# Kernel tuning notes

Hardware: AMD Instinct MI355X
Metric: run time of the kernel (lower is better)

## Reference

```python
import jax, jax.numpy as jnp
import numpy as np

UNITS = 2048
BATCH = 4096
INPUT_DIM = 2048

def hard_sigmoid(x):
    # Keras hard_sigmoid: clip(0.2*x + 0.5, 0, 1)
    return jnp.clip(0.2 * x + 0.5, 0.0, 1.0)

def setup_inputs() -> dict:
    key = jax.random.key(0)
    ks = jax.random.split(key, 8)
    inputs = jax.random.normal(ks[0], (BATCH, INPUT_DIM), dtype=jnp.float32)
    h_tm1 = jax.random.normal(ks[1], (BATCH, UNITS), dtype=jnp.float32)
    c_tm1 = jax.random.normal(ks[2], (BATCH, UNITS), dtype=jnp.float32)
    z_tm1 = jax.random.normal(ks[3], (BATCH, UNITS), dtype=jnp.float32)
    scale = 1.0 / np.sqrt(INPUT_DIM)
    kernel = jax.random.normal(ks[4], (INPUT_DIM, 4 * UNITS), dtype=jnp.float32) * scale
    recurrent_kernel = jax.random.normal(ks[5], (UNITS, 4 * UNITS), dtype=jnp.float32) * scale
    recurrent_latent = jax.random.normal(ks[6], (UNITS, 4 * UNITS), dtype=jnp.float32) * scale
    # unit_forget_bias: bias = [zeros(units), ones(units), zeros(2*units)]
    bias = jnp.concatenate([
        jnp.zeros((UNITS,), jnp.float32),
        jnp.ones((UNITS,), jnp.float32),
        jnp.zeros((2 * UNITS,), jnp.float32),
    ])
    return {"inputs": inputs, "h_tm1": h_tm1, "c_tm1": c_tm1, "z_tm1": z_tm1,
            "kernel": kernel, "recurrent_kernel": recurrent_kernel,
            "recurrent_latent": recurrent_latent, "bias": bias}

def reference(inputs, h_tm1, c_tm1, z_tm1, kernel, recurrent_kernel, recurrent_latent, bias):
    # Fused path (implementation=2, no dropout): three matmuls + bias,
    # split into 4 gates, then gated state update.
    x = inputs @ kernel + h_tm1 @ recurrent_kernel + z_tm1 @ recurrent_latent + bias
    x_i, x_f, x_c, x_o = jnp.split(x, 4, axis=1)
    i = hard_sigmoid(x_i)
    f = hard_sigmoid(x_f)
    c = f * c_tm1 + i * jnp.tanh(x_c)
    o = hard_sigmoid(x_o)
    h = o * jnp.tanh(c)
    return h
```

## Files before the change

kernel.cpp:

```cpp
#include <hip/hip_runtime.h>
#include <hip/hip_bf16.h>

typedef float f32x4 __attribute__((ext_vector_type(4)));
typedef short short8 __attribute__((ext_vector_type(8)));
typedef short short4v __attribute__((ext_vector_type(4)));

__device__ __forceinline__ short f2b(float x) {
    union { __hip_bfloat16 b; short s; } u;
    u.b = __float2bfloat16(x);
    return u.s;
}

__device__ __forceinline__ void gload16(const void* g, void* l) {
    __builtin_amdgcn_global_load_lds(
        (const __attribute__((address_space(1))) unsigned int*)g,
        (__attribute__((address_space(3))) unsigned int*)l, 16, 0, 0);
}

__global__ __launch_bounds__(256)
void conv_a(const float* __restrict__ x0, const float* __restrict__ x1,
            const float* __restrict__ x2, unsigned short* __restrict__ Aws)
{
    const long i = (long)blockIdx.x * 256 + threadIdx.x;
    const long per_src = (long)4096 * 2048 / 8;
    const int  s = (int)(i / per_src);
    const long e0 = (i % per_src) * 8;
    const int  row = (int)(e0 >> 11), kl = (int)(e0 & 2047);
    const float* src = (s == 0) ? x0 : (s == 1) ? x1 : x2;
    const f32x4 v0 = *(const f32x4*)(src + e0);
    const f32x4 v1 = *(const f32x4*)(src + e0 + 4);
    short8 p;
    #pragma unroll
    for (int j = 0; j < 4; ++j) { p[j] = f2b(v0[j]); p[4 + j] = f2b(v1[j]); }
    *(short8*)&Aws[(long)row * 6144 + s * 2048 + kl] = p;
}

__global__ __launch_bounds__(256)
void conv_b(const float* __restrict__ Wk, const float* __restrict__ Wr,
            const float* __restrict__ Wl, unsigned short* __restrict__ Bws)
{
    __shared__ float lt[64][65];
    const int bid = (int)blockIdx.x;
    const int s   = bid >> 12;
    const int r   = bid & 4095;
    const int kbase = (r >> 7) * 64;
    const int ebase = (r & 127) * 64;
    const float* W = (s == 0) ? Wk : (s == 1) ? Wr : Wl;
    const int tr = threadIdx.x >> 4, tc = threadIdx.x & 15;

    #pragma unroll
    for (int p = 0; p < 4; ++p) {
        const int kr = p * 16 + tr;
        const f32x4 v = *(const f32x4*)&W[(long)(kbase + kr) * 8192 + ebase + tc * 4];
        #pragma unroll
        for (int j = 0; j < 4; ++j) lt[kr][tc * 4 + j] = v[j];
    }
    __syncthreads();
    #pragma unroll
    for (int p = 0; p < 4; ++p) {
        const int er = p * 16 + tr;
        const int k4 = tc * 4;
        short4v qv;
        #pragma unroll
        for (int j = 0; j < 4; ++j) qv[j] = f2b(lt[k4 + j][er]);
        *(short4v*)&Bws[(long)(ebase + er) * 6144 + (long)s * 2048 + kbase + k4] = qv;
    }
}

__global__ __launch_bounds__(256, 2)
void vlstm_gemm8(const unsigned short* __restrict__ Aws,
                 const unsigned short* __restrict__ Bws,
                 const float* __restrict__ c_tm1,
                 const float* __restrict__ bias,
                 float* __restrict__ out)
{
    __shared__ __align__(16) unsigned short lds[2][2][128][64];

    const int tid  = threadIdx.x;
    const int w    = tid >> 6, lane = tid & 63;
    const int wm   = w >> 1,  wn   = w & 1;
    const int l15  = lane & 15, q = lane >> 4;
    const int lrow = lane >> 3;
    const int lsw  = (lane & 7) ^ lrow;
    const int oq   = q ^ (l15 & 7);

    const int bid = (int)blockIdx.x;
    const int swz = (bid & 7) * 256 + (bid >> 3);
    const int bm  = swz >> 6, bn = swz & 63;
    const int row0 = bm * 128, c0 = bn * 32;

    const long a_src0 = (long)(row0 + w * 32 + lrow) * 6144 + lsw * 8;
    const long b_src0 = (long)(c0 + w * 8 + lrow) * 6144 + lsw * 8;

    f32x4 acc[4][4];
    #pragma unroll
    for (int mi = 0; mi < 4; ++mi)
        #pragma unroll
        for (int g = 0; g < 4; ++g)
            acc[mi][g] = (f32x4){0.f, 0.f, 0.f, 0.f};

    short8 afr[4][2];
    short8 bfr[4][2];

#define STAGE_A(buf_, t_) do { _Pragma("unroll")                                 \
    for (int j_ = 0; j_ < 4; ++j_)                                               \
        gload16(Aws + a_src0 + (long)j_ * (8 * 6144) + (t_) * 64,                \
                &lds[buf_][0][w * 32 + j_ * 8][0]); } while (0)

#define STAGE_B(buf_, t_) do { _Pragma("unroll")                                 \
    for (int j_ = 0; j_ < 4; ++j_)    \
        gload16(Bws + b_src0 + (long)j_ * (2048 * 6144) + (t_) * 64,             \
                &lds[buf_][1][j_ * 32 + w * 8][0]); } while (0)

#define LOAD_AFR(cur_) do { _Pragma("unroll")                                    \
    for (int mi_ = 0; mi_ < 4; ++mi_) { _Pragma("unroll")                        \
        for (int h_ = 0; h_ < 2; ++h_)                                           \
            afr[mi_][h_] = *(const short8*)                                      \
                &lds[cur_][0][wm * 64 + mi_ * 16 + l15][(oq ^ (h_ << 2)) * 8];   \
    } } while (0)

#define LOAD_BFR(cur_, glo_) do { _Pragma("unroll")                              \
    for (int g_ = 0; g_ < 2; ++g_) { _Pragma("unroll")                           \
        for (int h_ = 0; h_ < 2; ++h_)                                           \
            bfr[(glo_) + g_][h_] = *(const short8*)                              \
                &lds[cur_][1][((glo_) + g_) * 32 + wn * 16 + l15]                \
                             [(oq ^ (h_ << 2)) * 8];                             \
    } } while (0)

#define MFMA_Q(glo_) do {                                                        \
    __builtin_amdgcn_s_setprio(1);                                               \
    _Pragma("unroll")                                                            \
    for (int h_ = 0; h_ < 2; ++h_) { _Pragma("unroll")                           \
        for (int mi_ = 0; mi_ < 4; ++mi_) { _Pragma("unroll")                    \
            for (int g_ = 0; g_ < 2; ++g_)                                       \
                acc[mi_][(glo_) + g_] = __builtin_amdgcn_mfma_f32_16x16x32_bf16( \
                    afr[mi_][h_], bfr[(glo_) + g_][h_], acc[mi_][(glo_) + g_],   \
                    0, 0, 0); } }                                                \
    __builtin_amdgcn_s_setprio(0); } while (0)

    STAGE_A(0, 0);
    STAGE_B(0, 0);
    asm volatile("s_waitcnt vmcnt(0)" ::: "memory");
    __builtin_amdgcn_s_barrier();
    __builtin_amdgcn_sched_barrier(0);

    for (int t = 0; t < 95; ++t) {
        const int cur = t & 1;
        STAGE_A(cur ^ 1, t + 1);
        LOAD_AFR(cur);
        LOAD_BFR(cur, 0);
        MFMA_Q(0);
        asm volatile("s_waitcnt vmcnt(4)" ::: "memory");
        __builtin_amdgcn_s_barrier();
        __builtin_amdgcn_sched_barrier(0);
        STAGE_B(cur ^ 1, t + 1);
        LOAD_BFR(cur, 2);
        MFMA_Q(2);
        asm volatile("s_waitcnt vmcnt(2)" ::: "memory");
        __builtin_amdgcn_s_barrier();
        __builtin_amdgcn_sched_barrier(0);
    }
    {
        const int cur = 95 & 1;
        LOAD_AFR(cur);
        LOAD_BFR(cur, 0);
        MFMA_Q(0);
        asm volatile("s_waitcnt vmcnt(0)" ::: "memory");
        __builtin_amdgcn_s_barrier();
        __builtin_amdgcn_sched_barrier(0);
        LOAD_BFR(cur, 2);
        MFMA_Q(2);
    }

#undef STAGE_A
#undef STAGE_B
#undef LOAD_AFR
#undef LOAD_BFR
#undef MFMA_Q

    {
        const int col = c0 + wn * 16 + l15;
        const float bi  = bias[col];
        const float bf_ = bias[2048 + col];
        const float bc  = bias[4096 + col];
        const float bo  = bias[6144 + col];
        #pragma unroll
        for (int mi = 0; mi < 4; ++mi) {
            const int rbase = row0 + wm * 64 + mi * 16 + q * 4;
            #pragma unroll
            for (int rr = 0; rr < 4; ++rr) {
                const int row = rbase + rr;
                const float xi = acc[mi][0][rr] + bi;
                const float xf = acc[mi][1][rr] + bf_;
                const float xc = acc[mi][2][rr] + bc;
                const float xo = acc[mi][3][rr] + bo;
                const float ig = __builtin_amdgcn_fmed3f(0.2f * xi + 0.5f, 0.f, 1.f);
                const float fg = __builtin_amdgcn_fmed3f(0.2f * xf + 0.5f, 0.f, 1.f);
                const float og = __builtin_amdgcn_fmed3f(0.2f * xo + 0.5f, 0.f, 1.f);
                const float cp = c_tm1[(long)row * 2048 + col];
                const float cc = fg * cp + ig * tanhf(xc);
                out[(long)row * 2048 + col] = og * tanhf(cc);
            }
        }
    }
}

__global__ __launch_bounds__(256, 2)
void vlstm_fused_legacy(const float* __restrict__ xin, const float* __restrict__ h_tm1,
                        const float* __restrict__ c_tm1, const float* __restrict__ z_tm1,
                        const float* __restrict__ Wk, const float* __restrict__ Wr,
                        const float* __restrict__ Wl, const float* __restrict__ bias,
                        float* __restrict__ out)
{
    __shared__ __align__(16) unsigned short Alds[2][128][40];
    __shared__ __align__(16) unsigned short Blds[2][256][40];

    const int tid  = threadIdx.x;
    const int wave = tid >> 6, lane = tid & 63;
    const int wr = wave >> 1, wc = wave & 1;
    const int l15 = lane & 15, q = lane >> 4;

    const int bid = (int)blockIdx.x;
    const int swz = (bid & 7) * 128 + (bid >> 3);
    const int bm = swz >> 5, bn = swz & 31;
    const int row0 = bm * 128, col0 = bn * 64;

    const int arow = tid >> 1, kh = tid & 1;
    const long bg_off = (long)(tid >> 6) * 2048 + col0 + (tid & 63);

    f32x4 acc[4][4][2];
    #pragma unroll
    for (int g = 0; g < 4; ++g)
        #pragma unroll
        for (int mi = 0; mi < 4; ++mi)
            #pragma unroll
            for (int ni = 0; ni < 2; ++ni)
                acc[g][mi][ni] = (f32x4){0.f, 0.f, 0.f, 0.f};

    f32x4 sa[4];
    float sb[32];

#define DO_LOADS_L(kn_) do {                                                    \
    const int s_  = (kn_) >> 6;                                                 \
    const int kl_ = ((kn_) & 63) << 5;                                          \
    const float* Ap_ = (s_ == 0) ? xin : (s_ == 1) ? h_tm1 : z_tm1;             \
    const float* Bp_ = (s_ == 0) ? Wk  : (s_ == 1) ? Wr    : Wl;                \
    const float* ap_ = Ap_ + (long)(row0 + arow) * 2048 + kl_ + kh * 16;        \
    _Pragma("unroll")                                                           \
    for (int i_ = 0; i_ < 4; ++i_) sa[i_] = ((const f32x4*)ap_)[i_];            \
    const float* bp_ = Bp_ + (long)kl_ * 8192 + bg_off;                         \
    _Pragma("unroll")                                                           \
    for (int kk_ = 0; kk_ < 32; ++kk_) sb[kk_] = bp_[(long)kk_ * 8192];         \
} while (0)

#define DO_STORE_L(buf_) do {                                                   \
    short8 p0_, p1_;                                                            \
    _Pragma("unroll")                                                           \
    for (int j_ = 0; j_ < 4; ++j_) {                                            \
        p0_[j_] = f2b(sa[0][j_]); p0_[4 + j_] = f2b(sa[1][j_]);                 \
        p1_[j_] = f2b(sa[2][j_]); p1_[4 + j_] = f2b(sa[3][j_]);                 \
    }                                                                           \
    *(short8*)&Alds[buf_][arow][kh * 16]     = p0_;                             \
    *(short8*)&Alds[buf_][arow][kh * 16 + 8] = p1_;                             \
    _Pragma("unroll")                                                           \
    for (int ks_ = 0; ks_ < 4; ++ks_) {                                         \
        short8 pb_;                                                             \
        _Pragma("unroll")                                                       \
        for (int j_ = 0; j_ < 8; ++j_) pb_[j_] = f2b(sb[ks_ * 8 + j_]);         \
        *(short8*)&Blds[buf_][tid][ks_ * 8] = pb_;                              \
    }                                                                           \
} while (0)

    DO_LOADS_L(0);
    DO_STORE_L(0);
    __syncthreads();

    for (int kt = 0; kt < 192; ++kt) {
        const int cur = kt & 1;
        if (kt + 1 < 192) DO_LOADS_L(kt + 1);

        short8 afr[4];
        #pragma unroll
        for (int mi = 0; mi < 4; ++mi)
            afr[mi] = *(const short8*)&Alds[cur][wr * 64 + mi * 16 + l15][q * 8];

        short8 bfr[4][2];
        #pragma unroll
        for (int g = 0; g < 4; ++g)
            #pragma unroll
            for (int ni = 0; ni < 2; ++ni)
                bfr[g][ni] = *(const short8*)
                    &Blds[cur][g * 64 + wc * 32 + ni * 16 + l15][q * 8];

        #pragma unroll
        for (int g = 0; g < 4; ++g)
            #pragma unroll
            for (int ni = 0; ni < 2; ++ni)
                #pragma unroll
                for (int mi = 0; mi < 4; ++mi)
                    acc[g][mi][ni] = __builtin_amdgcn_mfma_f32_16x16x32_bf16(
                        afr[mi], bfr[g][ni], acc[g][mi][ni], 0, 0, 0);

        if (kt + 1 < 192) DO_STORE_L(cur ^ 1);
        __syncthreads();
    }

#undef DO_LOADS_L
#undef DO_STORE_L

    #pragma unroll
    for (int ni = 0; ni < 2; ++ni) {
        const int col = col0 + wc * 32 + ni * 16 + l15;
        const float bi  = bias[col];
        const float bf_ = bias[2048 + col];
        const float bc  = bias[4096 + col];
        const float bo  = bias[6144 + col];
        #pragma unroll
        for (int mi = 0; mi < 4; ++mi) {
            const int rbase = row0 + wr * 64 + mi * 16 + q * 4;
            #pragma unroll
            for (int rr = 0; rr < 4; ++rr) {
                const int row = rbase + rr;
                const float xi = acc[0][mi][ni][rr] + bi;
                const float xf = acc[1][mi][ni][rr] + bf_;
                const float xc = acc[2][mi][ni][rr] + bc;
                const float xo = acc[3][mi][ni][rr] + bo;
                const float ig = __builtin_amdgcn_fmed3f(0.2f * xi + 0.5f, 0.f, 1.f);
                const float fg = __builtin_amdgcn_fmed3f(0.2f * xf + 0.5f, 0.f, 1.f);
                const float og = __builtin_amdgcn_fmed3f(0.2f * xo + 0.5f, 0.f, 1.f);
                const float cp = c_tm1[(long)row * 2048 + col];
                const float cc = fg * cp + ig * tanhf(xc);
                out[(long)row * 2048 + col] = og * tanhf(cc);
            }
        }
    }
}

extern "C" void kernel_launch(void* const* d_in, const int* in_sizes, int n_in,
                              void* d_out, int out_size, void* d_ws, size_t ws_size,
                              hipStream_t stream) {
    const float* xin  = (const float*)d_in[0];
    const float* h1   = (const float*)d_in[1];
    const float* c1   = (const float*)d_in[2];
    const float* z1   = (const float*)d_in[3];
    const float* Wk   = (const float*)d_in[4];
    const float* Wr   = (const float*)d_in[5];
    const float* Wl   = (const float*)d_in[6];
    const float* bias = (const float*)d_in[7];
    float* out = (float*)d_out;
    (void)in_sizes; (void)n_in; (void)out_size;

    const size_t a_elems = (size_t)4096 * 6144;
    const size_t b_elems = (size_t)8192 * 6144;
    const size_t need = (a_elems + b_elems) * 2;

    if (ws_size >= need) {
        unsigned short* Aws = (unsigned short*)d_ws;
        unsigned short* Bws = Aws + a_elems;
        conv_a<<<dim3(12288), dim3(256), 0, stream>>>(xin, h1, z1, Aws);
        conv_b<<<dim3(12288), dim3(256), 0, stream>>>(Wk, Wr, Wl, Bws);
        vlstm_gemm8<<<dim3(2048), dim3(256), 0, stream>>>(Aws, Bws, c1, bias, out);
    } else {
        vlstm_fused_legacy<<<dim3(1024), dim3(256), 0, stream>>>(
            xin, h1, c1, z1, Wk, Wr, Wl, bias, out);
    }
}
```

Baseline: 552.0 us.

## Enlarge GEMM tile to 256x256 with 8 waves and phased LDS pipeline

Replaces the 128-row by 32-unit (128 gate columns) block tile with a 256-row by 64-unit (256 gate columns) tile, run by 512 threads in 8 waves, each wave owning a 128x64 sub-tile. Staging of A and B into LDS is split across four barrier-delimited phases, and B is prefetched two iterations ahead. The aim is to raise arithmetic intensity and cut global/L2 traffic per MFMA. In exchange it uses more registers (acc[8][4]), LDS and barriers, and the launch drops to 512 blocks, which may hurt occupancy and load balance.

```diff
diff --git a/kernel.cpp b/kernel.cpp
--- a/kernel.cpp
+++ b/kernel.cpp
@@ -67,34 +67,34 @@
     }
 }
 
-__global__ __launch_bounds__(256, 2)
-void vlstm_gemm8(const unsigned short* __restrict__ Aws,
-                 const unsigned short* __restrict__ Bws,
-                 const float* __restrict__ c_tm1,
-                 const float* __restrict__ bias,
-                 float* __restrict__ out)
+__global__ __launch_bounds__(512, 2)
+void vlstm_gemm256(const unsigned short* __restrict__ Aws,
+                   const unsigned short* __restrict__ Bws,
+                   const float* __restrict__ c_tm1,
+                   const float* __restrict__ bias,
+                   float* __restrict__ out)
 {
-    __shared__ __align__(16) unsigned short lds[2][2][128][64];
+    __shared__ __align__(16) unsigned short As[2][256][64];
+    __shared__ __align__(16) unsigned short Bs[2][256][64];
 
     const int tid  = threadIdx.x;
     const int w    = tid >> 6, lane = tid & 63;
-    const int wm   = w >> 1,  wn   = w & 1;
+    const int wm   = w >> 2,  wn   = w & 3;
     const int l15  = lane & 15, q = lane >> 4;
     const int lrow = lane >> 3;
     const int lsw  = (lane & 7) ^ lrow;
     const int oq   = q ^ (l15 & 7);
 
     const int bid = (int)blockIdx.x;
-    const int swz = (bid & 7) * 256 + (bid >> 3);
-    const int bm  = swz >> 6, bn = swz & 63;
-    const int row0 = bm * 128, c0 = bn * 32;
-
-    const long a_src0 = (long)(row0 + w * 32 + lrow) * 6144 + lsw * 8;
-    const long b_src0 = (long)(c0 + w * 8 + lrow) * 6144 + lsw * 8;
-
-    f32x4 acc[4][4];
-    #pragma unroll
-    for (int mi = 0; mi < 4; ++mi)
+    const int swz = (bid & 7) * 64 + (bid >> 3);
+    const int bm  = swz >> 5, bn = swz & 31;
+    const int row0 = bm * 256, c0 = bn * 64;
+
+    const long a_base = (long)(row0 + w * 16 + lrow) * 6144 + lsw * 8;
+
+    f32x4 acc[8][4];
+    #pragma unroll
+    for (int mi = 0; mi < 8; ++mi)
         #pragma unroll
         for (int g = 0; g < 4; ++g)
             acc[mi][g] = (f32x4){0.f, 0.f, 0.f, 0.f};
@@ -102,74 +102,84 @@
     short8 afr[4][2];
     short8 bfr[4][2];
 
-#define STAGE_A(buf_, t_) do { _Pragma("unroll")                                 \
-    for (int j_ = 0; j_ < 4; ++j_)                                               \
-        gload16(Aws + a_src0 + (long)j_ * (8 * 6144) + (t_) * 64,                \
-                &lds[buf_][0][w * 32 + j_ * 8][0]); } while (0)
-
-#define STAGE_B(buf_, t_) do { _Pragma("unroll")                                 \
-    for (int j_ = 0; j_ < 4; ++j_)    \
-        gload16(Bws + b_src0 + (long)j_ * (2048 * 6144) + (t_) * 64,             \
-                &lds[buf_][1][j_ * 32 + w * 8][0]); } while (0)
-
-#define LOAD_AFR(cur_) do { _Pragma("unroll")                                    \
+#define STAGE_A(buf_, t_, h_) do { _Pragma("unroll")                             \
+    for (int j_ = 0; j_ < 2; ++j_)                                               \
+        gload16(Aws + a_base + (long)((h_) * 128 + j_ * 8) * 6144                \
+                    + (long)(t_) * 64,                                           \
+                &As[buf_][(h_) * 128 + w * 16 + j_ * 8][0]); } while (0)
+
+#define STAGE_B(buf_, t_, h_) do { _Pragma("unroll")                             \
+    for (int j_ = 0; j_ < 2; ++j_) {                                             \
+        const int e0_ = (h_) * 128 + w * 16 + j_ * 8;                            \
+        const int grow_ = ((e0_ >> 4) & 3) * 2048 + c0 + (e0_ >> 6) * 16         \
+                          + (e0_ & 8) + lrow;                                    \
+        gload16(Bws + (long)grow_ * 6144 + lsw * 8 + (long)(t_) * 64,            \
+                &Bs[buf_][e0_][0]); } } while (0)
+
+#define LOAD_AFR(cur_, mh_) do { _Pragma("unroll")                               \
     for (int mi_ = 0; mi_ < 4; ++mi_) { _Pragma("unroll")                        \
-        for (int h_ = 0; h_ < 2; ++h_)                                           \
-            afr[mi_][h_] = *(const short8*)                                      \
-                &lds[cur_][0][wm * 64 + mi_ * 16 + l15][(oq ^ (h_ << 2)) * 8];   \
-    } } while (0)
-
-#define LOAD_BFR(cur_, glo_) do { _Pragma("unroll")                              \
+        for (int kh_ = 0; kh_ < 2; ++kh_)                                        \
+            afr[mi_][kh_] = *(const short8*)                                     \
+                &As[cur_][wm * 128 + (mh_) * 64 + mi_ * 16 + l15]                \
+                         [(oq ^ (kh_ << 2)) * 8]; } } while (0)
+
+#define LOAD_BFR(cur_, nlo_) do { _Pragma("unroll")                              \
     for (int g_ = 0; g_ < 2; ++g_) { _Pragma("unroll")                           \
-        for (int h_ = 0; h_ < 2; ++h_)                                           \
-            bfr[(glo_) + g_][h_] = *(const short8*)                              \
-                &lds[cur_][1][((glo_) + g_) * 32 + wn * 16 + l15]                \
-                             [(oq ^ (h_ << 2)) * 8];                             \
-    } } while (0)
-
-#define MFMA_Q(glo_) do {                                                        \
+        for (int kh_ = 0; kh_ < 2; ++kh_)                                        \
+            bfr[(nlo_) + g_][kh_] = *(const short8*)                             \
+                &Bs[cur_][wn * 64 + ((nlo_) + g_) * 16 + l15]                    \
+                         [(oq ^ (kh_ << 2)) * 8]; } } while (0)
+
+#define MFMA_Q(mh_, nlo_) do {                                                   \
     __builtin_amdgcn_s_setprio(1);                                               \
     _Pragma("unroll")                                                            \
-    for (int h_ = 0; h_ < 2; ++h_) { _Pragma("unroll")                           \
+    for (int kh_ = 0; kh_ < 2; ++kh_) { _Pragma("unroll")                        \
         for (int mi_ = 0; mi_ < 4; ++mi_) { _Pragma("unroll")                    \
             for (int g_ = 0; g_ < 2; ++g_)                                       \
-                acc[mi_][(glo_) + g_] = __builtin_amdgcn_mfma_f32_16x16x32_bf16( \
-                    afr[mi_][h_], bfr[(glo_) + g_][h_], acc[mi_][(glo_) + g_],   \
-                    0, 0, 0); } }                                                \
+                acc[(mh_) * 4 + mi_][(nlo_) + g_] =                              \
+                    __builtin_amdgcn_mfma_f32_16x16x32_bf16(                     \
+                        afr[mi_][kh_], bfr[(nlo_) + g_][kh_],                    \
+                        acc[(mh_) * 4 + mi_][(nlo_) + g_], 0, 0, 0); } }         \
     __builtin_amdgcn_s_setprio(0); } while (0)
 
-    STAGE_A(0, 0);
-    STAGE_B(0, 0);
-    asm volatile("s_waitcnt vmcnt(0)" ::: "memory");
+#define PH_OPEN() do { __builtin_amdgcn_s_barrier();                             \
+    asm volatile("s_waitcnt lgkmcnt(0)" ::: "memory");                           \
+    __builtin_amdgcn_sched_barrier(0); } while (0)
+
+#define PH_CLOSE() do { __builtin_amdgcn_s_barrier();                            \
+    __builtin_amdgcn_sched_barrier(0); } while (0)
+
+    STAGE_A(0, 0, 0); STAGE_A(0, 0, 1);
+    STAGE_B(0, 0, 0); STAGE_B(0, 0, 1);
+    STAGE_B(1, 1, 0); STAGE_B(1, 1, 1);
+    asm volatile("s_waitcnt vmcnt(4)" ::: "memory");
     __builtin_amdgcn_s_barrier();
     __builtin_amdgcn_sched_barrier(0);
 
-    for (int t = 0; t < 95; ++t) {
-        const int cur = t & 1;
-        STAGE_A(cur ^ 1, t + 1);
-        LOAD_AFR(cur);
+    for (int t = 0; t < 96; ++t) {
+        const int cur = t & 1, nxt = cur ^ 1;
+        LOAD_AFR(cur, 0);
         LOAD_BFR(cur, 0);
-        MFMA_Q(0);
-        asm volatile("s_waitcnt vmcnt(4)" ::: "memory");
-        __builtin_amdgcn_s_barrier();
-        __builtin_amdgcn_sched_barrier(0);
-        STAGE_B(cur ^ 1, t + 1);
+        if (t + 1 < 96) STAGE_A(nxt, t + 1, 0);
+        PH_OPEN();
+        MFMA_Q(0, 0);
+        PH_CLOSE();
         LOAD_BFR(cur, 2);
-        MFMA_Q(2);
-        asm volatile("s_waitcnt vmcnt(2)" ::: "memory");
-        __builtin_amdgcn_s_barrier();
-        __builtin_amdgcn_sched_barrier(0);
-    }
-    {
-        const int cur = 95 & 1;
-        LOAD_AFR(cur);
-        LOAD_BFR(cur, 0);
-        MFMA_Q(0);
-        asm volatile("s_waitcnt vmcnt(0)" ::: "memory");
-        __builtin_amdgcn_s_barrier();
-        __builtin_amdgcn_sched_barrier(0);
-        LOAD_BFR(cur, 2);
-        MFMA_Q(2);
+        if (t + 1 < 96) STAGE_A(nxt, t + 1, 1);
+        PH_OPEN();
+        MFMA_Q(0, 2);
+        PH_CLOSE();
+        LOAD_AFR(cur, 1);
+        if (t + 2 < 96) STAGE_B(cur, t + 2, 0);
+        PH_OPEN();
+        MFMA_Q(1, 0);
+        PH_CLOSE();
+        if (t + 2 < 96) STAGE_B(cur, t + 2, 1);
+        PH_OPEN();
+        MFMA_Q(1, 2);
+        if (t < 94) asm volatile("s_waitcnt vmcnt(4)" ::: "memory");
+        else        asm volatile("s_waitcnt vmcnt(0)" ::: "memory");
+        PH_CLOSE();
     }
 
 #undef STAGE_A
@@ -177,6 +187,8 @@
 #undef LOAD_AFR
 #undef LOAD_BFR
 #undef MFMA_Q
+#undef PH_OPEN
+#undef PH_CLOSE
 
     {
         const int col = c0 + wn * 16 + l15;
@@ -185,8 +197,8 @@
         const float bc  = bias[4096 + col];
         const float bo  = bias[6144 + col];
         #pragma unroll
-        for (int mi = 0; mi < 4; ++mi) {
-            const int rbase = row0 + wm * 64 + mi * 16 + q * 4;
+        for (int mi = 0; mi < 8; ++mi) {
+            const int rbase = row0 + wm * 128 + mi * 16 + q * 4;
             #pragma unroll
             for (int rr = 0; rr < 4; ++rr) {
                 const int row = rbase + rr;
@@ -359,7 +371,7 @@
         unsigned short* Bws = Aws + a_elems;
         conv_a<<<dim3(12288), dim3(256), 0, stream>>>(xin, h1, z1, Aws);
         conv_b<<<dim3(12288), dim3(256), 0, stream>>>(Wk, Wr, Wl, Bws);
-        vlstm_gemm8<<<dim3(2048), dim3(256), 0, stream>>>(Aws, Bws, c1, bias, out);
+        vlstm_gemm256<<<dim3(512), dim3(512), 0, stream>>>(Aws, Bws, c1, bias, out);
     } else {
         vlstm_fused_legacy<<<dim3(1024), dim3(256), 0, stream>>>(
             xin, h1, c1, z1, Wk, Wr, Wl, bias, out);
```

After: 508.3 us. 7.9% less time.
